# Performance work log

Hardware: AMD Instinct MI355X
Metric: run time of the kernel (lower is better)

The kernel has to match this reference:

```python
import jax, jax.numpy as jnp
import numpy as np

N_LAYERS = 3
NUM_NODES = 400000
EMB_DIM = 64
N_EDGES = 4000000


def setup_inputs() -> dict:
    key = jax.random.key(0)
    k1, k2, k3, k4 = jax.random.split(key, 4)
    embedding = jax.random.normal(k1, (NUM_NODES, EMB_DIM), dtype=jnp.float32) * 0.1
    adj_row = jax.random.randint(k2, (N_EDGES,), 0, NUM_NODES, dtype=jnp.int64)
    adj_col = jax.random.randint(k3, (N_EDGES,), 0, NUM_NODES, dtype=jnp.int64)
    # normalized adjacency values (e.g. 1/sqrt(d_i d_j)); positive, small
    adj_val = jax.random.uniform(k4, (N_EDGES,), dtype=jnp.float32) * 0.01
    return {"embedding": embedding, "adj_row": adj_row, "adj_col": adj_col, "adj_val": adj_val}


def _spmm(row, col, val, x):
    # sparse [N,N] @ dense [N,D]: gather neighbor rows, scale, scatter-add
    msgs = val[:, None] * x[col]                      # [E, D]
    return jax.ops.segment_sum(msgs, row, num_segments=NUM_NODES)


def reference(embedding, adj_row, adj_col, adj_val):
    # LightGCN propagation: running mean over layer outputs (fused accumulator,
    # mathematically identical to stack+mean over n_layers+1 embeddings)
    x = embedding
    acc = x
    for _ in range(N_LAYERS):
        x = _spmm(adj_row, adj_col, adj_val, x)
        acc = acc + x
    all_embeddings = acc / jnp.asarray(N_LAYERS + 1, dtype=x.dtype)
    return all_embeddings
```

## Files before the change

kernel.cpp:

```cpp
#include <hip/hip_runtime.h>

#define EMB 64
#define SCAN_B 256
#define RPB 32
#define RPW 8
#define ECAP 1024

typedef unsigned uint2v __attribute__((ext_vector_type(2)));
typedef float float4v __attribute__((ext_vector_type(4)));
typedef int int4v __attribute__((ext_vector_type(4)));

__device__ inline uint2 nt_load_u2(const uint2* p) {
    uint2v v = __builtin_nontemporal_load((const uint2v*)p);
    return make_uint2(v.x, v.y);
}
__device__ inline void nt_store_u2(uint2* p, uint2 v) {
    uint2v t; t.x = v.x; t.y = v.y;
    __builtin_nontemporal_store(t, (uint2v*)p);
}
__device__ inline float4 nt_load_f4(const float4* p) {
    float4v v = __builtin_nontemporal_load((const float4v*)p);
    return make_float4(v.x, v.y, v.z, v.w);
}
__device__ inline void nt_store_f4(float4* p, float4 v) {
    float4v t; t.x = v.x; t.y = v.y; t.z = v.z; t.w = v.w;
    __builtin_nontemporal_store(t, (float4v*)p);
}

__device__ inline unsigned short f2bf(float f) {
    unsigned u = __float_as_uint(f);
    return (unsigned short)((u + 0x7fffu + ((u >> 16) & 1u)) >> 16);
}
__device__ inline float bl(unsigned u) { return __uint_as_float(u << 16); }
__device__ inline float bh(unsigned u) { return __uint_as_float(u & 0xffff0000u); }


__global__ void zero_ints(int* __restrict__ p, int n) {
    int i = blockIdx.x * blockDim.x + threadIdx.x;
    if (i < n) p[i] = 0;
}

__global__ void hist_rows(const int* __restrict__ row, int* __restrict__ S, int E) {
    int e = blockIdx.x * blockDim.x + threadIdx.x;
    if (e < E) atomicAdd(&S[__builtin_nontemporal_load(row + e)], 1);
}

__global__ void hist_rows4(const int* __restrict__ row, int* __restrict__ S, int E4) {
    int i = blockIdx.x * blockDim.x + threadIdx.x;
    if (i < E4) {
        int4v r = __builtin_nontemporal_load((const int4v*)row + i);
        atomicAdd(&S[r.x], 1);
        atomicAdd(&S[r.y], 1);
        atomicAdd(&S[r.z], 1);
        atomicAdd(&S[r.w], 1);
    }
}

__global__ void scan_block_sums(const int* __restrict__ S, int* __restrict__ bsum, int N) {
    __shared__ int sdata[SCAN_B];
    int i = blockIdx.x * SCAN_B + threadIdx.x;
    sdata[threadIdx.x] = (i < N) ? S[i] : 0;
    __syncthreads();
    for (int off = SCAN_B / 2; off > 0; off >>= 1) {
        if (threadIdx.x < off) sdata[threadIdx.x] += sdata[threadIdx.x + off];
        __syncthreads();
    }
    if (threadIdx.x == 0) bsum[blockIdx.x] = sdata[0];
}

__global__ void scan_sums(int* __restrict__ bsum, int nb) {
    __shared__ int part[1024];
    int t = threadIdx.x;
    int i0 = 2 * t, i1 = 2 * t + 1;
    int a = (i0 < nb) ? bsum[i0] : 0;
    int b = (i1 < nb) ? bsum[i1] : 0;
    part[t] = a + b;
    __syncthreads();
    for (int off = 1; off < 1024; off <<= 1) {
        int v = part[t];
        int add = (t >= off) ? part[t - off] : 0;
        __syncthreads();
        part[t] = v + add;
        __syncthreads();
    }
    int excl = (t == 0) ? 0 : part[t - 1];
    if (i0 < nb) bsum[i0] = excl;
    if (i1 < nb) bsum[i1] = excl + a;
}

__global__ void scan_apply(int* __restrict__ S, const int* __restrict__ bsum, int N) {
    __shared__ int sdata[SCAN_B];
    int i = blockIdx.x * SCAN_B + threadIdx.x;
    int v = (i < N) ? S[i] : 0;
    sdata[threadIdx.x] = v;
    __syncthreads();
    for (int off = 1; off < SCAN_B; off <<= 1) {
        int val = sdata[threadIdx.x];
        int add = (threadIdx.x >= off) ? sdata[threadIdx.x - off] : 0;
        __syncthreads();
        sdata[threadIdx.x] = val + add;
        __syncthreads();
    }
    int excl = (threadIdx.x == 0 ? 0 : sdata[threadIdx.x - 1]) + bsum[blockIdx.x];
    if (i < N) S[i] = excl;
}

__global__ void scatter_edges_ranged(const int* __restrict__ row, const int* __restrict__ col,
                                     const float* __restrict__ val,
                                     int* __restrict__ S, uint2* __restrict__ epack,
                                     int E, int rstep) {
    int pass  = blockIdx.x & 7;
    int chunk = blockIdx.x >> 3;
    int e = chunk * blockDim.x + threadIdx.x;
    if (e >= E) return;
    int r = __builtin_nontemporal_load(row + e);
    int lo = pass * rstep;
    if (r < lo || r >= lo + rstep) return;
    int c = __builtin_nontemporal_load(col + e);
    float v = __builtin_nontemporal_load(val + e);
    int pos = atomicAdd(&S[r], 1);
    epack[pos] = make_uint2((unsigned)c, __float_as_uint(v));
}

__global__ void conv_bf16(const float4* __restrict__ src, uint2* __restrict__ dst, int n4) {
    int i = blockIdx.x * blockDim.x + threadIdx.x;
    if (i < n4) {
        float4 v = nt_load_f4(src + i);
        unsigned w0 = (unsigned)f2bf(v.x) | ((unsigned)f2bf(v.y) << 16);
        unsigned w1 = (unsigned)f2bf(v.z) | ((unsigned)f2bf(v.w) << 16);
        nt_store_u2(dst + i, make_uint2(w0, w1));
    }
}

template<bool STG>
__device__ __forceinline__ void spmm_rows(
    const uint2* __restrict__ epack, const uint2* __restrict__ esh, int beg0,
    const int* __restrict__ Ssh, int j0,
    const unsigned short* __restrict__ x, const float* __restrict__ emb,
    const uint2* __restrict__ x1b, const uint2* __restrict__ x2b,
    unsigned short* __restrict__ y, float* __restrict__ acc,
    int rb, int N, int mode, int lane, int grp, int d4)
{
    const uint2 z2 = make_uint2(0u, 0u);

#define EDG(i) (STG ? esh[(i) - beg0] : epack[i])
#define LOADR(J, B_, E_, P0, P1, P2, P3, G0, G1, G2, G3)                         \
    {                                                                            \
        B_ = Ssh[J]; E_ = Ssh[(J) + 1];                                          \
        int i0 = B_ + grp, i1 = i0 + 4, i2 = i0 + 8, i3 = i0 + 12;               \
        P0 = (i0 < E_) ? EDG(i0) : z2;                                           \
        P1 = (i1 < E_) ? EDG(i1) : z2;                                           \
        P2 = (i2 < E_) ? EDG(i2) : z2;                                           \
        P3 = (i3 < E_) ? EDG(i3) : z2;                                           \
        G0 = (i0 < E_) ? ((const uint2*)(x + ((size_t)P0.x << 6)))[d4] : z2;     \
        G1 = (i1 < E_) ? ((const uint2*)(x + ((size_t)P1.x << 6)))[d4] : z2;     \
        G2 = (i2 < E_) ? ((const uint2*)(x + ((size_t)P2.x << 6)))[d4] : z2;     \
        G3 = (i3 < E_) ? ((const uint2*)(x + ((size_t)P3.x << 6)))[d4] : z2;     \
    }

    int aB = 0, aE = 0;
    uint2 ap0 = z2, ap1 = z2, ap2 = z2, ap3 = z2, ag0 = z2, ag1 = z2, ag2 = z2, ag3 = z2;
    int bB = 0, bE = 0;
    uint2 bp0 = z2, bp1 = z2, bp2 = z2, bp3 = z2, bg0 = z2, bg1 = z2, bg2 = z2, bg3 = z2;

    LOADR(j0, aB, aE, ap0, ap1, ap2, ap3, ag0, ag1, ag2, ag3);

    for (int k = 0; k < RPW; ++k) {
        int j = j0 + k;
        int r = rb + j;
        if (k + 1 < RPW) {
            LOADR(j + 1, bB, bE, bp0, bp1, bp2, bp3, bg0, bg1, bg2, bg3);
        }

        float4 s = make_float4(0.f, 0.f, 0.f, 0.f);
        {
            int i0 = aB + grp, i1 = i0 + 4, i2 = i0 + 8, i3 = i0 + 12;
            float w0 = (i0 < aE) ? __uint_as_float(ap0.y) : 0.f;
            float w1 = (i1 < aE) ? __uint_as_float(ap1.y) : 0.f;
            float w2 = (i2 < aE) ? __uint_as_float(ap2.y) : 0.f;
            float w3 = (i3 < aE) ? __uint_as_float(ap3.y) : 0.f;
            s.x += w0 * bl(ag0.x); s.y += w0 * bh(ag0.x); s.z += w0 * bl(ag0.y); s.w += w0 * bh(ag0.y);
            s.x += w1 * bl(ag1.x); s.y += w1 * bh(ag1.x); s.z += w1 * bl(ag1.y); s.w += w1 * bh(ag1.y);
            s.x += w2 * bl(ag2.x); s.y += w2 * bh(ag2.x); s.z += w2 * bl(ag2.y); s.w += w2 * bh(ag2.y);
            s.x += w3 * bl(ag3.x); s.y += w3 * bh(ag3.x); s.z += w3 * bl(ag3.y); s.w += w3 * bh(ag3.y);
        }
        for (int base = aB + 16; base < aE; base += 16) {
            int i0 = base + grp, i1 = i0 + 4, i2 = i0 + 8, i3 = i0 + 12;
            uint2 p0 = (i0 < aE) ? EDG(i0) : z2;
            uint2 p1 = (i1 < aE) ? EDG(i1) : z2;
            uint2 p2 = (i2 < aE) ? EDG(i2) : z2;
            uint2 p3 = (i3 < aE) ? EDG(i3) : z2;
            uint2 g0 = (i0 < aE) ? ((const uint2*)(x + ((size_t)p0.x << 6)))[d4] : z2;
            uint2 g1 = (i1 < aE) ? ((const uint2*)(x + ((size_t)p1.x << 6)))[d4] : z2;
            uint2 g2 = (i2 < aE) ? ((const uint2*)(x + ((size_t)p2.x << 6)))[d4] : z2;
            uint2 g3 = (i3 < aE) ? ((const uint2*)(x + ((size_t)p3.x << 6)))[d4] : z2;
            float w0 = (i0 < aE) ? __uint_as_float(p0.y) : 0.f;
            float w1 = (i1 < aE) ? __uint_as_float(p1.y) : 0.f;
            float w2 = (i2 < aE) ? __uint_as_float(p2.y) : 0.f;
            float w3 = (i3 < aE) ? __uint_as_float(p3.y) : 0.f;
            s.x += w0 * bl(g0.x); s.y += w0 * bh(g0.x); s.z += w0 * bl(g0.y); s.w += w0 * bh(g0.y);
            s.x += w1 * bl(g1.x); s.y += w1 * bh(g1.x); s.z += w1 * bl(g1.y); s.w += w1 * bh(g1.y);
            s.x += w2 * bl(g2.x); s.y += w2 * bh(g2.x); s.z += w2 * bl(g2.y); s.w += w2 * bh(g2.y);
            s.x += w3 * bl(g3.x); s.y += w3 * bh(g3.x); s.z += w3 * bl(g3.y); s.w += w3 * bh(g3.y);
        }

        s.x += __shfl_xor(s.x, 32); s.y += __shfl_xor(s.y, 32);
        s.z += __shfl_xor(s.z, 32); s.w += __shfl_xor(s.w, 32);
        s.x += __shfl_xor(s.x, 16); s.y += __shfl_xor(s.y, 16);
        s.z += __shfl_xor(s.z, 16); s.w += __shfl_xor(s.w, 16);

        if (lane < 16 && r < N) {
            size_t o4 = (size_t)r * 16 + d4;
            if (mode != 2) {
                unsigned w0 = (unsigned)f2bf(s.x) | ((unsigned)f2bf(s.y) << 16);
                unsigned w1 = (unsigned)f2bf(s.z) | ((unsigned)f2bf(s.w) << 16);
                nt_store_u2(((uint2*)y) + o4, make_uint2(w0, w1));
            } else {
                float4 e4 = nt_load_f4(((const float4*)emb) + o4);
                uint2 a1 = nt_load_u2(x1b + o4);
                uint2 a2 = nt_load_u2(x2b + o4);
                float rx = e4.x + bl(a1.x) + bl(a2.x) + s.x;
                float ry = e4.y + bh(a1.x) + bh(a2.x) + s.y;
                float rz = e4.z + bl(a1.y) + bl(a2.y) + s.z;
                float rw = e4.w + bh(a1.y) + bh(a2.y) + s.w;
                nt_store_f4(((float4*)acc) + o4,
                            make_float4(rx * 0.25f, ry * 0.25f, rz * 0.25f, rw * 0.25f));
            }
        }
        aB = bB; aE = bE;
        ap0 = bp0; ap1 = bp1; ap2 = bp2; ap3 = bp3;
        ag0 = bg0; ag1 = bg1; ag2 = bg2; ag3 = bg3;
    }
#undef LOADR
#undef EDG
}

__global__ __launch_bounds__(256) void spmm_csr2(
    const uint2* __restrict__ epack, const int* __restrict__ S,
    const unsigned short* __restrict__ x, const float* __restrict__ emb,
    const uint2* __restrict__ x1b, const uint2* __restrict__ x2b,
    unsigned short* __restrict__ y, float* __restrict__ acc,
    int N, int mode)
{
    __shared__ int Ssh[RPB + 1];
    __shared__ uint2 esh[ECAP];

    int tid = threadIdx.x;
    int rb = blockIdx.x * RPB;

    if (tid <= RPB) {
        int rr = rb - 1 + tid;
        Ssh[tid] = (rr < 0) ? 0 : S[rr < N ? rr : (N - 1)];
    }
    __syncthreads();

    int beg0 = Ssh[0];
    int nE = Ssh[RPB] - beg0;
    bool staged = (nE <= ECAP);
    if (staged) {
        for (int i = tid; i < nE; i += 256) esh[i] = nt_load_u2(epack + beg0 + i);
    }
    __syncthreads();

    int wid = tid >> 6, lane = tid & 63;
    int grp = lane >> 4, d4 = lane & 15;
    int j0 = wid * RPW;

    if (staged)
        spmm_rows<true >(epack, esh, beg0, Ssh, j0, x, emb, x1b, x2b, y, acc, rb, N, mode, lane, grp, d4);
    else
        spmm_rows<false>(epack, esh, beg0, Ssh, j0, x, emb, x1b, x2b, y, acc, rb, N, mode, lane, grp, d4);
}


__global__ void lgcn_init(const float4* __restrict__ emb, float4* __restrict__ A,
                          float4* __restrict__ acc, float4* __restrict__ B, int n4) {
    int i = blockIdx.x * blockDim.x + threadIdx.x;
    if (i < n4) { float4 v = emb[i]; A[i] = v; acc[i] = v; B[i] = make_float4(0,0,0,0); }
}
__global__ void lgcn_spmm(const int* __restrict__ row, const int* __restrict__ col,
                          const float* __restrict__ val, const float* __restrict__ x,
                          float* __restrict__ y, int E) {
    int gid = blockIdx.x * blockDim.x + threadIdx.x;
    int e = gid >> 6;
    if (e >= E) return;
    int d = threadIdx.x & 63;
    atomicAdd(y + (size_t)row[e] * EMB + d, val[e] * x[(size_t)col[e] * EMB + d]);
}
__global__ void lgcn_addzero(float4* __restrict__ acc, const float4* __restrict__ X,
                             float4* __restrict__ Y, int n4) {
    int i = blockIdx.x * blockDim.x + threadIdx.x;
    if (i < n4) {
        float4 a = acc[i]; float4 xv = X[i];
        a.x += xv.x; a.y += xv.y; a.z += xv.z; a.w += xv.w;
        acc[i] = a; Y[i] = make_float4(0,0,0,0);
    }
}
__global__ void lgcn_final(float4* __restrict__ acc, const float4* __restrict__ X, int n4) {
    int i = blockIdx.x * blockDim.x + threadIdx.x;
    if (i < n4) {
        float4 a = acc[i]; float4 xv = X[i];
        a.x = (a.x + xv.x) * 0.25f; a.y = (a.y + xv.y) * 0.25f;
        a.z = (a.z + xv.z) * 0.25f; a.w = (a.w + xv.w) * 0.25f;
        acc[i] = a;
    }
}

extern "C" void kernel_launch(void* const* d_in, const int* in_sizes, int n_in,
                              void* d_out, int out_size, void* d_ws, size_t ws_size,
                              hipStream_t stream) {
    const float* emb = (const float*)d_in[0];
    const int*   row = (const int*)d_in[1];
    const int*   col = (const int*)d_in[2];
    const float* val = (const float*)d_in[3];
    float* acc = (float*)d_out;

    const int N = in_sizes[0] / EMB;
    const int E = in_sizes[1];
    const int TB = 256;

    const size_t buf_elems = (size_t)N * EMB;
    const int nb = (N + SCAN_B - 1) / SCAN_B;

    const size_t need = (size_t)E * 8 + buf_elems * 2 * 3 + (size_t)N * 4 + (size_t)nb * 4;

    if (ws_size >= need) {
        uint2* epack = (uint2*)d_ws;
        unsigned short* X0 = (unsigned short*)(epack + E);
        unsigned short* X1 = X0 + buf_elems;
        unsigned short* X2 = X1 + buf_elems;
        int* S    = (int*)(X2 + buf_elems);
        int* bsum = S + N;

        const int eb  = (E + TB - 1) / TB;
        const int nbN = (N + TB - 1) / TB;
        const int n4  = (int)(buf_elems / 4);
        const int cvb = (n4 + TB - 1) / TB;
        const int spmm_blocks = (N + RPB - 1) / RPB;
        const int rstep = (N + 7) / 8;

        zero_ints<<<nbN, TB, 0, stream>>>(S, N);
        if ((E & 3) == 0) {
            const int e4b = (E / 4 + TB - 1) / TB;
            hist_rows4<<<e4b, TB, 0, stream>>>(row, S, E / 4);
        } else {
            hist_rows<<<eb, TB, 0, stream>>>(row, S, E);
        }
        scan_block_sums<<<nb, SCAN_B, 0, stream>>>(S, bsum, N);
        scan_sums<<<1, 1024, 0, stream>>>(bsum, nb);
        scan_apply<<<nb, SCAN_B, 0, stream>>>(S, bsum, N);
        scatter_edges_ranged<<<eb * 8, TB, 0, stream>>>(row, col, val, S, epack, E, rstep);
        conv_bf16<<<cvb, TB, 0, stream>>>((const float4*)emb, (uint2*)X0, n4);

        spmm_csr2<<<spmm_blocks, TB, 0, stream>>>(epack, S, X0, nullptr, nullptr, nullptr,
                                                  X1, nullptr, N, 0);
        spmm_csr2<<<spmm_blocks, TB, 0, stream>>>(epack, S, X1, nullptr, nullptr, nullptr,
                                                  X2, nullptr, N, 1);
        spmm_csr2<<<spmm_blocks, TB, 0, stream>>>(epack, S, X2, emb,
                                                  (const uint2*)X1, (const uint2*)X2,
                                                  nullptr, acc, N, 2);
    } else {
        float* A = (float*)d_ws;
        float* B = A + buf_elems;
        const int n4 = (int)(buf_elems / 4);
        const int ew_blocks = (n4 + TB - 1) / TB;
        const int spmm_blocks = (E + 3) / 4;
        lgcn_init<<<ew_blocks, TB, 0, stream>>>((const float4*)emb, (float4*)A,
                                                (float4*)acc, (float4*)B, n4);
        lgcn_spmm<<<spmm_blocks, TB, 0, stream>>>(row, col, val, A, B, E);
        lgcn_addzero<<<ew_blocks, TB, 0, stream>>>((float4*)acc, (const float4*)B,
                                                   (float4*)A, n4);
        lgcn_spmm<<<spmm_blocks, TB, 0, stream>>>(row, col, val, B, A, E);
        lgcn_addzero<<<ew_blocks, TB, 0, stream>>>((float4*)acc, (const float4*)A,
                                                   (float4*)B, n4);
        lgcn_spmm<<<spmm_blocks, TB, 0, stream>>>(row, col, val, A, B, E);
        lgcn_final<<<ew_blocks, TB, 0, stream>>>((float4*)acc, (const float4*)B, n4);
    }
}
```

Before: 982.2 us.

## Replace multi-pass ranged edge scatter with two-phase bucketed partition

Edges are first partitioned in one pass into per-group, per-1024-row buckets in a scratch region reused from an intermediate buffer, then each bucket is scattered into CSR order with localized atomics. This removes the 8 repeated passes over the row array and the globally scattered writes of the old scatter. Bucket overflow falls back to direct atomic placement. The final layer also reads the bf16 copy of the embedding instead of the fp32 original, trading a little precision for less bandwidth.

```diff
diff --git a/kernel.cpp b/kernel.cpp
--- a/kernel.cpp
+++ b/kernel.cpp
@@ -5,6 +5,8 @@
 #define RPB 32
 #define RPW 8
 #define ECAP 1024
+#define BW_SH 10
+#define SEGCAP 1536
 
 typedef unsigned uint2v __attribute__((ext_vector_type(2)));
 typedef float float4v __attribute__((ext_vector_type(4)));
@@ -103,6 +105,49 @@
     }
     int excl = (threadIdx.x == 0 ? 0 : sdata[threadIdx.x - 1]) + bsum[blockIdx.x];
     if (i < N) S[i] = excl;
+}
+
+__global__ void partition_edges(const int* __restrict__ row, const int* __restrict__ col,
+                                const float* __restrict__ val,
+                                int* __restrict__ C, uint2* __restrict__ tmp,
+                                int* __restrict__ S, uint2* __restrict__ epack,
+                                int E, int NB) {
+    int e = blockIdx.x * blockDim.x + threadIdx.x;
+    if (e >= E) return;
+    int g = blockIdx.x & 7;
+    int r = __builtin_nontemporal_load(row + e);
+    int c = __builtin_nontemporal_load(col + e);
+    float v = __builtin_nontemporal_load(val + e);
+    int b = r >> BW_SH;
+    int seg = g * NB + b;
+    int idx = atomicAdd(&C[seg], 1);
+    if (idx < SEGCAP) {
+        tmp[(size_t)seg * SEGCAP + idx] =
+            make_uint2((unsigned)c | ((unsigned)(r & ((1 << BW_SH) - 1)) << 19),
+                       __float_as_uint(v));
+    } else {
+        int pos = atomicAdd(&S[r], 1);
+        epack[pos] = make_uint2((unsigned)c, __float_as_uint(v));
+    }
+}
+
+__global__ void scatter_bucketed(const int* __restrict__ C, const uint2* __restrict__ tmp,
+                                 int* __restrict__ S, uint2* __restrict__ epack, int NB) {
+    int b = blockIdx.x;
+    int rb = b << BW_SH;
+    for (int g = 0; g < 8; ++g) {
+        int seg = g * NB + b;
+        int cnt = C[seg];
+        if (cnt > SEGCAP) cnt = SEGCAP;
+        size_t base = (size_t)seg * SEGCAP;
+        for (int i = threadIdx.x; i < cnt; i += blockDim.x) {
+            uint2 t = nt_load_u2(tmp + base + i);
+            int r = rb + (int)(t.x >> 19);
+            unsigned c = t.x & 0x7FFFFu;
+            int pos = atomicAdd(&S[r], 1);
+            epack[pos] = make_uint2(c, t.y);
+        }
+    }
 }
 
 __global__ void scatter_edges_ranged(const int* __restrict__ row, const int* __restrict__ col,
@@ -136,8 +181,8 @@
 __device__ __forceinline__ void spmm_rows(
     const uint2* __restrict__ epack, const uint2* __restrict__ esh, int beg0,
     const int* __restrict__ Ssh, int j0,
-    const unsigned short* __restrict__ x, const float* __restrict__ emb,
-    const uint2* __restrict__ x1b, const uint2* __restrict__ x2b,
+    const unsigned short* __restrict__ x,
+    const uint2* __restrict__ x0b, const uint2* __restrict__ x1b, const uint2* __restrict__ x2b,
     unsigned short* __restrict__ y, float* __restrict__ acc,
     int rb, int N, int mode, int lane, int grp, int d4)
 {
@@ -216,13 +261,13 @@
                 unsigned w1 = (unsigned)f2bf(s.z) | ((unsigned)f2bf(s.w) << 16);
                 nt_store_u2(((uint2*)y) + o4, make_uint2(w0, w1));
             } else {
-                float4 e4 = nt_load_f4(((const float4*)emb) + o4);
+                uint2 a0 = nt_load_u2(x0b + o4);
                 uint2 a1 = nt_load_u2(x1b + o4);
                 uint2 a2 = nt_load_u2(x2b + o4);
-                float rx = e4.x + bl(a1.x) + bl(a2.x) + s.x;
-                float ry = e4.y + bh(a1.x) + bh(a2.x) + s.y;
-                float rz = e4.z + bl(a1.y) + bl(a2.y) + s.z;
-                float rw = e4.w + bh(a1.y) + bh(a2.y) + s.w;
+                float rx = bl(a0.x) + bl(a1.x) + bl(a2.x) + s.x;
+                float ry = bh(a0.x) + bh(a1.x) + bh(a2.x) + s.y;
+                float rz = bl(a0.y) + bl(a1.y) + bl(a2.y) + s.z;
+                float rw = bh(a0.y) + bh(a1.y) + bh(a2.y) + s.w;
                 nt_store_f4(((float4*)acc) + o4,
                             make_float4(rx * 0.25f, ry * 0.25f, rz * 0.25f, rw * 0.25f));
             }
@@ -237,8 +282,8 @@
 
 __global__ __launch_bounds__(256) void spmm_csr2(
     const uint2* __restrict__ epack, const int* __restrict__ S,
-    const unsigned short* __restrict__ x, const float* __restrict__ emb,
-    const uint2* __restrict__ x1b, const uint2* __restrict__ x2b,
+    const unsigned short* __restrict__ x,
+    const uint2* __restrict__ x0b, const uint2* __restrict__ x1b, const uint2* __restrict__ x2b,
     unsigned short* __restrict__ y, float* __restrict__ acc,
     int N, int mode)
 {
@@ -267,9 +312,9 @@
     int j0 = wid * RPW;
 
     if (staged)
-        spmm_rows<true >(epack, esh, beg0, Ssh, j0, x, emb, x1b, x2b, y, acc, rb, N, mode, lane, grp, d4);
+        spmm_rows<true >(epack, esh, beg0, Ssh, j0, x, x0b, x1b, x2b, y, acc, rb, N, mode, lane, grp, d4);
     else
-        spmm_rows<false>(epack, esh, beg0, Ssh, j0, x, emb, x1b, x2b, y, acc, rb, N, mode, lane, grp, d4);
+        spmm_rows<false>(epack, esh, beg0, Ssh, j0, x, x0b, x1b, x2b, y, acc, rb, N, mode, lane, grp, d4);
 }
 
 
@@ -337,7 +382,6 @@
         const int n4  = (int)(buf_elems / 4);
         const int cvb = (n4 + TB - 1) / TB;
         const int spmm_blocks = (N + RPB - 1) / RPB;
-        const int rstep = (N + 7) / 8;
 
         zero_ints<<<nbN, TB, 0, stream>>>(S, N);
         if ((E & 3) == 0) {
@@ -349,15 +393,30 @@
         scan_block_sums<<<nb, SCAN_B, 0, stream>>>(S, bsum, N);
         scan_sums<<<1, 1024, 0, stream>>>(bsum, nb);
         scan_apply<<<nb, SCAN_B, 0, stream>>>(S, bsum, N);
-        scatter_edges_ranged<<<eb * 8, TB, 0, stream>>>(row, col, val, S, epack, E, rstep);
+
+        const int NB = (N + (1 << BW_SH) - 1) >> BW_SH;
+        const size_t tmp_bytes = (size_t)8 * NB * SEGCAP * 8;
+        bool bucketed = (N < (1 << 19)) &&
+                        (tmp_bytes + (size_t)8 * NB * 4 <= buf_elems * 2 * 2);
+        if (bucketed) {
+            uint2* tmp = (uint2*)X1;
+            int* C = (int*)((char*)X1 + tmp_bytes);
+            const int cb = (8 * NB + TB - 1) / TB;
+            zero_ints<<<cb, TB, 0, stream>>>(C, 8 * NB);
+            partition_edges<<<eb, TB, 0, stream>>>(row, col, val, C, tmp, S, epack, E, NB);
+            scatter_bucketed<<<NB, TB, 0, stream>>>(C, tmp, S, epack, NB);
+        } else {
+            const int rstep = (N + 7) / 8;
+            scatter_edges_ranged<<<eb * 8, TB, 0, stream>>>(row, col, val, S, epack, E, rstep);
+        }
         conv_bf16<<<cvb, TB, 0, stream>>>((const float4*)emb, (uint2*)X0, n4);
 
         spmm_csr2<<<spmm_blocks, TB, 0, stream>>>(epack, S, X0, nullptr, nullptr, nullptr,
                                                   X1, nullptr, N, 0);
         spmm_csr2<<<spmm_blocks, TB, 0, stream>>>(epack, S, X1, nullptr, nullptr, nullptr,
                                                   X2, nullptr, N, 1);
-        spmm_csr2<<<spmm_blocks, TB, 0, stream>>>(epack, S, X2, emb,
-                                                  (const uint2*)X1, (const uint2*)X2,
+        spmm_csr2<<<spmm_blocks, TB, 0, stream>>>(epack, S, X2,
+                                                  (const uint2*)X0, (const uint2*)X1, (const uint2*)X2,
                                                   nullptr, acc, N, 2);
     } else {
         float* A = (float*)d_ws;
```

Measured after the change: 1.289 ms. 31.3% more time.
